# Kernel tuning notes

Measured on AMD Instinct MI355X. Metric: run time of the kernel, lower is better.

## Reference

```python
import jax, jax.numpy as jnp
import numpy as np

B, N, D, U, S = 32, 1024, 2, 64, 2


def setup_inputs() -> dict:
    key = jax.random.key(0)
    ks = jax.random.split(key, 8)
    scale = 1.0 / np.sqrt(N)  # keep diffusion outputs in a sane range
    inputs = jax.random.normal(ks[0], (B, N, D), jnp.float32)
    supports = jax.random.normal(ks[1], (B, N, N, S), jnp.float32) * scale
    h_prev = jax.random.normal(ks[2], (B, N * U), jnp.float32)
    rows = (D + U) * (S + 1)  # 198
    wscale = 1.0 / np.sqrt(rows)
    r_kernel = jax.random.normal(ks[3], (rows, U), jnp.float32) * wscale
    u_kernel = jax.random.normal(ks[4], (rows, U), jnp.float32) * wscale
    c_kernel = jax.random.normal(ks[5], (rows, U), jnp.float32) * wscale
    zeros = jnp.zeros((U,), jnp.float32)
    return {"inputs": inputs, "supports": supports, "h_prev": h_prev,
            "r_kernel": r_kernel, "r_bias": zeros,
            "u_kernel": u_kernel, "u_bias": zeros,
            "c_kernel": c_kernel, "c_bias": zeros}


def _diff_conv(x_in, supports, state, kernel, bias):
    # x_in: (B,N,D), state: (B, N*U) -> output (B, N*U)
    b, n, _ = x_in.shape
    u = kernel.shape[1]
    x0 = jnp.concatenate([x_in, state.reshape(b, n, u)], axis=-1)  # (B,N,F)
    # batched graph diffusion for all S supports at once: (B,N,N,S)x(B,N,F)->(B,N,F,S)
    xm = jnp.einsum('bijs,bjf->bifs', supports, x0)
    x = jnp.concatenate([x0[..., None], xm], axis=-1)  # (B,N,F,M) matches tf stack+transpose order
    x = x.reshape(b * n, -1) @ kernel + bias  # (B*N, U)
    return x.reshape(b, n * u)


def reference(inputs, supports, h_prev, r_kernel, r_bias, u_kernel, u_bias, c_kernel, c_bias):
    r = jax.nn.sigmoid(_diff_conv(inputs, supports, h_prev, r_kernel, r_bias))
    u = jax.nn.sigmoid(_diff_conv(inputs, supports, h_prev, u_kernel, u_bias))
    c = jnp.tanh(_diff_conv(inputs, supports, r * h_prev, c_kernel, c_bias))
    h = u * h_prev + (1.0 - u) * c
    return h
```

## Files before the change

kernel.cpp:

```cpp
#include <hip/hip_runtime.h>
#include <hip/hip_bf16.h>

namespace {

constexpr int kN  = 1024;
constexpr int kU  = 64;
constexpr int kFP = 80;
constexpr int kXR = 132;

typedef __attribute__((ext_vector_type(4))) float f32x4;
typedef __attribute__((ext_vector_type(8))) short sv8;
typedef unsigned int u32;
typedef unsigned short u16;

__device__ __forceinline__ u32 pack_bf2(float a, float b) {
  __hip_bfloat16 ha = __float2bfloat16(a);
  __hip_bfloat16 hb = __float2bfloat16(b);
  u16 ua = *reinterpret_cast<u16*>(&ha);
  u16 ub = *reinterpret_cast<u16*>(&hb);
  return (u32)ua | ((u32)ub << 16);
}

__device__ __forceinline__ u16 bf16bits(float a) {
  __hip_bfloat16 h = __float2bfloat16(a);
  return *reinterpret_cast<u16*>(&h);
}

__device__ __forceinline__ float bflo(u32 v) {
  u32 x = v << 16;
  return *reinterpret_cast<float*>(&x);
}
__device__ __forceinline__ float bfhi(u32 v) {
  u32 x = v & 0xffff0000u;
  return *reinterpret_cast<float*>(&x);
}

__device__ __forceinline__ void gl16(const void* g, void* l) {
  __builtin_amdgcn_global_load_lds(
      (const __attribute__((address_space(1))) u32*)g,
      (__attribute__((address_space(3))) u32*)l, 16, 0, 0);
}

__global__ __launch_bounds__(256) void build_x0t(
    const float* __restrict__ inputs, const float* __restrict__ h_prev,
    __hip_bfloat16* __restrict__ x0t, __hip_bfloat16* __restrict__ x0tc) {
  const int bx = blockIdx.x;
  const int b  = bx >> 4;
  const int n0 = (bx & 15) * 64;
  const int t  = threadIdx.x;

  __shared__ float hp[64][65];

  const float* hpg = h_prev + (size_t)b * kN * kU + (size_t)n0 * kU;
#pragma unroll
  for (int r = 0; r < 16; ++r) {
    int idx = t + (r << 8);
    hp[idx >> 6][idx & 63] = hpg[idx];
  }
  __syncthreads();

  {
    int u = t >> 2, g = t & 3;
    __hip_bfloat16* dst = x0t + ((size_t)b * kFP + 2 + u) * kN + n0 + g * 16;
#pragma unroll
    for (int k = 0; k < 16; ++k) dst[k] = __float2bfloat16(hp[g * 16 + k][u]);
  }

  if (t < 128) {
    int d = t & 1, nn = t >> 1;
    float v = inputs[((size_t)b * kN + n0 + nn) * 2 + d];
    __hip_bfloat16 bv = __float2bfloat16(v);
    x0t [((size_t)b * kFP + d) * kN + n0 + nn] = bv;
    x0tc[((size_t)b * kFP + d) * kN + n0 + nn] = bv;
  } else {
    int i2 = t - 128;
    __hip_bfloat16 z = __float2bfloat16(0.0f);
#pragma unroll
    for (int r = 0; r < 7; ++r) {
      int idx = i2 + r * 128;
      int row = 66 + (idx >> 6), nn = idx & 63;
      x0t [((size_t)b * kFP + row) * kN + n0 + nn] = z;
      x0tc[((size_t)b * kFP + row) * kN + n0 + nn] = z;
    }
  }
}

__global__ __launch_bounds__(512, 4) void einsum_diff(
    const float* __restrict__ sup, const __hip_bfloat16* __restrict__ x0t,
    u16* __restrict__ xfeat) {
  const int bx = blockIdx.x;
  const int wk = (bx & 7) * 64 + (bx >> 3);
  const int b  = wk >> 4;
  const int i0 = (wk & 15) << 6;
  const int t    = threadIdx.x;
  const int lane = t & 63;
  const int w    = t >> 6;
  const int q    = lane >> 4;
  const int lm   = lane & 15;
  const int s    = w & 1;
  const int ih   = w >> 1;

  __shared__ u16 Af[2][2][2][4][64][8];
  __shared__ u16 Xf[2][10][64][8];

  f32x4 acc[5];
#pragma unroll
  for (int n = 0; n < 5; ++n) acc[n] = (f32x4){0.f, 0.f, 0.f, 0.f};

  const float* sbase = sup + ((size_t)b * kN + i0) * (kN * 2);
  const u16* xg = reinterpret_cast<const u16*>(x0t) + (size_t)b * kFP * kN;

  const int ii = t >> 3, jb = t & 7;
  const float* aSrc = sbase + (size_t)ii * (kN * 2) + jb * 16;
  const int ksA = jb >> 2, q2 = jb & 3;
  const int ihhA = ii >> 4, lm2 = ii & 15;
  const int aOff = ksA * 4096 + ihhA * 1024 +
                   ((((q2 * 16 + lm2) * 16)) ^ (q2 << 4) ^ (ksA << 6));
  char* const afBase = (char*)&Af[0][0][0][0][0][0];

  const int seg1 = w;
  const int seg2 = w + 8;
  const u16* xs1;
  const u16* xs2 = nullptr;
  {
    int k1 = seg1 / 5, n1 = seg1 % 5;
    xs1 = xg + (size_t)(n1 * 16 + lm) * kN + k1 * 32 + q * 8;
    if (w < 2) {
      int k2 = seg2 / 5, n2 = seg2 % 5;
      xs2 = xg + (size_t)(n2 * 16 + lm) * kN + k2 * 32 + q * 8;
    }
  }

  float4 R[4];

  auto dmaX = [&](int nb, int T) {
    int jo = T * 64;
    gl16(xs1 + jo, &Xf[nb][seg1][0][0]);
    if (w < 2) gl16(xs2 + jo, &Xf[nb][seg2][0][0]);
  };

  auto loadA = [&](int T) {
    const float* p = aSrc + T * 128;
    R[0] = *reinterpret_cast<const float4*>(p);
    R[1] = *reinterpret_cast<const float4*>(p + 4);
    R[2] = *reinterpret_cast<const float4*>(p + 8);
    R[3] = *reinterpret_cast<const float4*>(p + 12);
  };

  auto packWrite = [&](int nb) {
    u32 p0[4], p1[4];
#pragma unroll
    for (int r = 0; r < 4; ++r) {
      p0[r] = pack_bf2(R[r].x, R[r].z);
      p1[r] = pack_bf2(R[r].y, R[r].w);
    }
    char* base = afBase + nb * 16384 + aOff;
    *reinterpret_cast<uint4*>(base)        = *reinterpret_cast<uint4*>(p0);
    *reinterpret_cast<uint4*>(base + 8192) = *reinterpret_cast<uint4*>(p1);
  };

  auto compute = [&](int cb_) {
#pragma unroll
    for (int ks = 0; ks < 2; ++ks) {
      const char* ab = afBase + cb_ * 16384 + s * 8192 + ks * 4096 + ih * 1024;
      sv8 a = *reinterpret_cast<const sv8*>(
          ab + ((((q * 16 + lm) * 16)) ^ (q << 4) ^ (ks << 6)));
#pragma unroll
      for (int n = 0; n < 5; ++n) {
        sv8 xb = *reinterpret_cast<const sv8*>(&Xf[cb_][ks * 5 + n][lane][0]);
        acc[n] = __builtin_amdgcn_mfma_f32_16x16x32_bf16(a, xb, acc[n], 0, 0, 0);
      }
    }
  };

  dmaX(0, 0);
  loadA(0);
  asm volatile("s_waitcnt vmcnt(0)" ::: "memory");
  packWrite(0);
  asm volatile("s_waitcnt lgkmcnt(0)" ::: "memory");
  __builtin_amdgcn_s_barrier();
  __builtin_amdgcn_sched_barrier(0);

#pragma unroll 1
  for (int T = 0; T < 15; ++T) {
    const int nb = (T + 1) & 1;
    dmaX(nb, T + 1);
    loadA(T + 1);
    compute(T & 1);
    asm volatile("s_waitcnt vmcnt(0)" ::: "memory");
    packWrite(nb);
    asm volatile("s_waitcnt lgkmcnt(0)" ::: "memory");
    __builtin_amdgcn_s_barrier();
    __builtin_amdgcn_sched_barrier(0);
  }
  compute(1);
  __syncthreads();

  u16* ep = (u16*)afBase;
#pragma unroll
  for (int n = 0; n < 5; ++n) {
    int f = n * 16 + lm;
    if (f < 66) {
#pragma unroll
      for (int r = 0; r < 4; ++r) {
        int row = ih * 16 + q * 4 + r;
        ep[row * 136 + s * 66 + f] = bf16bits(acc[n][r]);
      }
    }
  }
  __syncthreads();
  const u32* ep32 = (const u32*)afBase;
  u32* og = reinterpret_cast<u32*>(xfeat) + ((size_t)b * kN + i0) * 66;
#pragma unroll 1
  for (int g = t; g < 4224; g += 512) {
    int row = g / 66, c = g - row * 66;
    og[g] = ep32[row * 68 + c];
  }
}

__global__ __launch_bounds__(256) void gates_ru(
    const u16* __restrict__ xfeat, const float* __restrict__ rk,
    const float* __restrict__ rbias, const float* __restrict__ uk,
    const float* __restrict__ ubias, const float* __restrict__ inputs,
    const float* __restrict__ h_prev, float* __restrict__ u_buf,
    __hip_bfloat16* __restrict__ x0tc) {
  const int row0 = blockIdx.x * 32;
  const int b = row0 >> 10, n0 = row0 & 1023;
  const int t = threadIdx.x;
  __shared__ float xm[32][134];
  __shared__ float x0s[32][66];

  {
    const u32* xsrc = reinterpret_cast<const u32*>(xfeat) + (size_t)row0 * 66;
#pragma unroll 1
    for (int g = t; g < 2112; g += 256) {
      int row = g / 66, c = g - row * 66;
      u32 v = xsrc[g];
      xm[row][c * 2]     = bflo(v);
      xm[row][c * 2 + 1] = bfhi(v);
    }
  }
#pragma unroll
  for (int r2 = 0; r2 < 8; ++r2) {
    int idx = t + (r2 << 8);
    int rw = idx >> 6, u = idx & 63;
    x0s[rw][2 + u] = h_prev[(size_t)(row0 + rw) * kU + u];
  }
  if (t < 64) x0s[t >> 1][t & 1] = inputs[(size_t)row0 * 2 + t];
  __syncthreads();

  const int cu = t & 15;
  const int rw = (t >> 4) * 2;
  float ar[2][4] = {{0.f,0.f,0.f,0.f},{0.f,0.f,0.f,0.f}};
  float au[2][4] = {{0.f,0.f,0.f,0.f},{0.f,0.f,0.f,0.f}};

#pragma unroll 4
  for (int f = 0; f < 66; ++f) {
    float4 vr = *reinterpret_cast<const float4*>(rk + (size_t)(f * 3) * kU + cu * 4);
    float4 vu = *reinterpret_cast<const float4*>(uk + (size_t)(f * 3) * kU + cu * 4);
    float a0 = x0s[rw][f], a1 = x0s[rw + 1][f];
    ar[0][0] += a0 * vr.x; ar[0][1] += a0 * vr.y; ar[0][2] += a0 * vr.z; ar[0][3] += a0 * vr.w;
    ar[1][0] += a1 * vr.x; ar[1][1] += a1 * vr.y; ar[1][2] += a1 * vr.z; ar[1][3] += a1 * vr.w;
    au[0][0] += a0 * vu.x; au[0][1] += a0 * vu.y; au[0][2] += a0 * vu.z; au[0][3] += a0 * vu.w;
    au[1][0] += a1 * vu.x; au[1][1] += a1 * vu.y; au[1][2] += a1 * vu.z; au[1][3] += a1 * vu.w;
  }
#pragma unroll
  for (int m = 1; m <= 2; ++m) {
#pragma unroll 4
    for (int f = 0; f < 66; ++f) {
      float4 vr = *reinterpret_cast<const float4*>(rk + (size_t)(f * 3 + m) * kU + cu * 4);
      float4 vu = *reinterpret_cast<const float4*>(uk + (size_t)(f * 3 + m) * kU + cu * 4);
      float a0 = xm[rw][(m - 1) * 66 + f], a1 = xm[rw + 1][(m - 1) * 66 + f];
      ar[0][0] += a0 * vr.x; ar[0][1] += a0 * vr.y; ar[0][2] += a0 * vr.z; ar[0][3] += a0 * vr.w;
      ar[1][0] += a1 * vr.x; ar[1][1] += a1 * vr.y; ar[1][2] += a1 * vr.z; ar[1][3] += a1 * vr.w;
      au[0][0] += a0 * vu.x; au[0][1] += a0 * vu.y; au[0][2] += a0 * vu.z; au[0][3] += a0 * vu.w;
      au[1][0] += a1 * vu.x; au[1][1] += a1 * vu.y; au[1][2] += a1 * vu.z; au[1][3] += a1 * vu.w;
    }
  }

#pragma unroll
  for (int rr = 0; rr < 2; ++rr) {
    int grow = row0 + rw + rr;
    int n = n0 + rw + rr;
#pragma unroll
    for (int j = 0; j < 4; ++j) {
      int u = cu * 4 + j;
      float rv = 1.f / (1.f + __expf(-(ar[rr][j] + rbias[u])));
      float uv = 1.f / (1.f + __expf(-(au[rr][j] + ubias[u])));
      u_buf[(size_t)grow * kU + u] = uv;
      float rh = rv * h_prev[(size_t)grow * kU + u];
      x0tc[((size_t)b * kFP + 2 + u) * kN + n] = __float2bfloat16(rh);
    }
  }
}

__global__ __launch_bounds__(256) void gate_c_final(
    const u16* __restrict__ xfeat, const float* __restrict__ ck,
    const float* __restrict__ cbias, const float* __restrict__ inputs,
    const __hip_bfloat16* __restrict__ x0tc, const float* __restrict__ h_prev,
    const float* __restrict__ u_buf, float* __restrict__ out) {
  const int row0 = blockIdx.x * 32;
  const int b = row0 >> 10, n0 = row0 & 1023;
  const int t = threadIdx.x;
  __shared__ float xm[32][134];
  __shared__ float x0c[32][66];

  {
    const u32* xsrc = reinterpret_cast<const u32*>(xfeat) + (size_t)row0 * 66;
#pragma unroll 1
    for (int g = t; g < 2112; g += 256) {
      int row = g / 66, c = g - row * 66;
      u32 v = xsrc[g];
      xm[row][c * 2]     = bflo(v);
      xm[row][c * 2 + 1] = bfhi(v);
    }
  }
#pragma unroll
  for (int r2 = 0; r2 < 8; ++r2) {
    int idx = t + (r2 << 8);
    int u = idx >> 5, nn = idx & 31;
    x0c[nn][2 + u] =
        __bfloat162float(x0tc[((size_t)b * kFP + 2 + u) * kN + n0 + nn]);
  }
  if (t < 64) x0c[t >> 1][t & 1] = inputs[(size_t)row0 * 2 + t];
  __syncthreads();

  const int cu = t & 15;
  const int rw = (t >> 4) * 2;
  float ac[2][4] = {{0.f,0.f,0.f,0.f},{0.f,0.f,0.f,0.f}};

#pragma unroll 4
  for (int f = 0; f < 66; ++f) {
    float4 vc = *reinterpret_cast<const float4*>(ck + (size_t)(f * 3) * kU + cu * 4);
    float a0 = x0c[rw][f], a1 = x0c[rw + 1][f];
    ac[0][0] += a0 * vc.x; ac[0][1] += a0 * vc.y; ac[0][2] += a0 * vc.z; ac[0][3] += a0 * vc.w;
    ac[1][0] += a1 * vc.x; ac[1][1] += a1 * vc.y; ac[1][2] += a1 * vc.z; ac[1][3] += a1 * vc.w;
  }
#pragma unroll
  for (int m = 1; m <= 2; ++m) {
#pragma unroll 4
    for (int f = 0; f < 66; ++f) {
      float4 vc = *reinterpret_cast<const float4*>(ck + (size_t)(f * 3 + m) * kU + cu * 4);
      float a0 = xm[rw][(m - 1) * 66 + f], a1 = xm[rw + 1][(m - 1) * 66 + f];
      ac[0][0] += a0 * vc.x; ac[0][1] += a0 * vc.y; ac[0][2] += a0 * vc.z; ac[0][3] += a0 * vc.w;
      ac[1][0] += a1 * vc.x; ac[1][1] += a1 * vc.y; ac[1][2] += a1 * vc.z; ac[1][3] += a1 * vc.w;
    }
  }

#pragma unroll
  for (int rr = 0; rr < 2; ++rr) {
    int grow = row0 + rw + rr;
#pragma unroll
    for (int j = 0; j < 4; ++j) {
      int u = cu * 4 + j;
      float cv = tanhf(ac[rr][j] + cbias[u]);
      float uv = u_buf[(size_t)grow * kU + u];
      float hp = h_prev[(size_t)grow * kU + u];
      out[(size_t)grow * kU + u] = uv * hp + (1.f - uv) * cv;
    }
  }
}

}

extern "C" void kernel_launch(void* const* d_in, const int* in_sizes, int n_in,
                              void* d_out, int out_size, void* d_ws, size_t ws_size,
                              hipStream_t stream) {
  const float* inputs = (const float*)d_in[0];
  const float* sup    = (const float*)d_in[1];
  const float* h_prev = (const float*)d_in[2];
  const float* rk     = (const float*)d_in[3];
  const float* rbias  = (const float*)d_in[4];
  const float* uk     = (const float*)d_in[5];
  const float* ubias  = (const float*)d_in[6];
  const float* ck     = (const float*)d_in[7];
  const float* cbias  = (const float*)d_in[8];
  float* out = (float*)d_out;

  char* ws = (char*)d_ws;
  __hip_bfloat16* x0t   = (__hip_bfloat16*)(ws);
  __hip_bfloat16* x0tc  = (__hip_bfloat16*)(ws + 5242880);
  u16*            xfeat = (u16*)(ws + 10485760);
  float*          u_buf = (float*)(ws + 19136512);

  hipLaunchKernelGGL(build_x0t, dim3(512), dim3(256), 0, stream,
                     inputs, h_prev, x0t, x0tc);
  hipLaunchKernelGGL(einsum_diff, dim3(512), dim3(512), 0, stream,
                     sup, x0t, xfeat);
  hipLaunchKernelGGL(gates_ru, dim3(1024), dim3(256), 0, stream,
                     xfeat, rk, rbias, uk, ubias, inputs, h_prev, u_buf, x0tc);
  hipLaunchKernelGGL(einsum_diff, dim3(512), dim3(512), 0, stream,
                     sup, x0tc, xfeat);
  hipLaunchKernelGGL(gate_c_final, dim3(1024), dim3(256), 0, stream,
                     xfeat, ck, cbias, inputs, x0tc, h_prev, u_buf, out);
}
```

Before: 232.6 us.

## Load einsum operands straight into registers and drop LDS staging and barriers

Rewrites the diffusion einsum kernel so each wave loads its own rows of supports and the x0 tile directly from global memory into registers, double-buffered across k-steps, and converts them to bf16 MFMA fragments in registers. Both supports go through the same wave, which removes the shared-memory staging of A and X and the per-iteration barriers. Blocks shrink to 256 threads, and each wave now covers 16 rows with two accumulator sets. The trade-off is that neighbouring waves no longer share X through LDS, so X is re-read redundantly from cache. Register pressure also rises, which may lower occupancy.

New measurement: 266.4 us. +14.5%, slower.

```diff
diff --git a/kernel.cpp b/kernel.cpp
--- a/kernel.cpp
+++ b/kernel.cpp
@@ -6,10 +6,10 @@
 constexpr int kN  = 1024;
 constexpr int kU  = 64;
 constexpr int kFP = 80;
-constexpr int kXR = 132;
 
 typedef __attribute__((ext_vector_type(4))) float f32x4;
 typedef __attribute__((ext_vector_type(8))) short sv8;
+typedef __attribute__((ext_vector_type(4))) unsigned u32x4;
 typedef unsigned int u32;
 typedef unsigned short u16;
 
@@ -33,12 +33,6 @@
 __device__ __forceinline__ float bfhi(u32 v) {
   u32 x = v & 0xffff0000u;
   return *reinterpret_cast<float*>(&x);
-}
-
-__device__ __forceinline__ void gl16(const void* g, void* l) {
-  __builtin_amdgcn_global_load_lds(
-      (const __attribute__((address_space(1))) u32*)g,
-      (__attribute__((address_space(3))) u32*)l, 16, 0, 0);
 }
 
 __global__ __launch_bounds__(256) void build_x0t(
@@ -85,134 +79,100 @@
   }
 }
 
-__global__ __launch_bounds__(512, 4) void einsum_diff(
+__global__ __launch_bounds__(256, 2) void einsum_diff(
     const float* __restrict__ sup, const __hip_bfloat16* __restrict__ x0t,
     u16* __restrict__ xfeat) {
   const int bx = blockIdx.x;
   const int wk = (bx & 7) * 64 + (bx >> 3);
-  const int b  = wk >> 4;
-  const int i0 = (wk & 15) << 6;
   const int t    = threadIdx.x;
   const int lane = t & 63;
   const int w    = t >> 6;
   const int q    = lane >> 4;
   const int lm   = lane & 15;
-  const int s    = w & 1;
-  const int ih   = w >> 1;
-
-  __shared__ u16 Af[2][2][2][4][64][8];
-  __shared__ u16 Xf[2][10][64][8];
-
-  f32x4 acc[5];
-#pragma unroll
-  for (int n = 0; n < 5; ++n) acc[n] = (f32x4){0.f, 0.f, 0.f, 0.f};
-
-  const float* sbase = sup + ((size_t)b * kN + i0) * (kN * 2);
-  const u16* xg = reinterpret_cast<const u16*>(x0t) + (size_t)b * kFP * kN;
-
-  const int ii = t >> 3, jb = t & 7;
-  const float* aSrc = sbase + (size_t)ii * (kN * 2) + jb * 16;
-  const int ksA = jb >> 2, q2 = jb & 3;
-  const int ihhA = ii >> 4, lm2 = ii & 15;
-  const int aOff = ksA * 4096 + ihhA * 1024 +
-                   ((((q2 * 16 + lm2) * 16)) ^ (q2 << 4) ^ (ksA << 6));
-  char* const afBase = (char*)&Af[0][0][0][0][0][0];
-
-  const int seg1 = w;
-  const int seg2 = w + 8;
-  const u16* xs1;
-  const u16* xs2 = nullptr;
-  {
-    int k1 = seg1 / 5, n1 = seg1 % 5;
-    xs1 = xg + (size_t)(n1 * 16 + lm) * kN + k1 * 32 + q * 8;
-    if (w < 2) {
-      int k2 = seg2 / 5, n2 = seg2 % 5;
-      xs2 = xg + (size_t)(n2 * 16 + lm) * kN + k2 * 32 + q * 8;
-    }
-  }
-
-  float4 R[4];
-
-  auto dmaX = [&](int nb, int T) {
-    int jo = T * 64;
-    gl16(xs1 + jo, &Xf[nb][seg1][0][0]);
-    if (w < 2) gl16(xs2 + jo, &Xf[nb][seg2][0][0]);
+
+  const int gw  = wk * 4 + w;
+  const int b   = gw >> 6;
+  const int i0w = (gw & 63) * 16;
+  const int i0b = ((wk * 4) & 63) * 16;
+
+  __shared__ u16 ep[64][136];
+
+  f32x4 acc[2][5];
+#pragma unroll
+  for (int s_ = 0; s_ < 2; ++s_)
+#pragma unroll
+    for (int n = 0; n < 5; ++n) acc[s_][n] = (f32x4){0.f, 0.f, 0.f, 0.f};
+
+  const float* aB = sup + ((size_t)b * kN + i0w + lm) * (kN * 2) + q * 16;
+  const u16* xg2 = reinterpret_cast<const u16*>(x0t) +
+                   (size_t)b * kFP * kN + (size_t)lm * kN + q * 8;
+
+  sv8   XP[10], XQ[10];
+  float4 AP[8], AQ[8];
+
+  auto issue = [&](sv8 (&X)[10], float4 (&A)[8], int T) {
+#pragma unroll
+    for (int ks = 0; ks < 2; ++ks) {
+#pragma unroll
+      for (int r = 0; r < 4; ++r)
+        A[ks * 4 + r] = *reinterpret_cast<const float4*>(
+            aB + T * 128 + ks * 64 + r * 4);
+#pragma unroll
+      for (int n = 0; n < 5; ++n)
+        X[ks * 5 + n] = *reinterpret_cast<const sv8*>(
+            xg2 + (size_t)n * 16 * kN + ks * 32 + T * 64);
+    }
   };
 
-  auto loadA = [&](int T) {
-    const float* p = aSrc + T * 128;
-    R[0] = *reinterpret_cast<const float4*>(p);
-    R[1] = *reinterpret_cast<const float4*>(p + 4);
-    R[2] = *reinterpret_cast<const float4*>(p + 8);
-    R[3] = *reinterpret_cast<const float4*>(p + 12);
+  auto step = [&](const sv8 (&X)[10], const float4 (&A)[8]) {
+#pragma unroll
+    for (int ks = 0; ks < 2; ++ks) {
+      u32 w0[4], w1[4];
+#pragma unroll
+      for (int r = 0; r < 4; ++r) {
+        w0[r] = pack_bf2(A[ks * 4 + r].x, A[ks * 4 + r].z);
+        w1[r] = pack_bf2(A[ks * 4 + r].y, A[ks * 4 + r].w);
+      }
+      sv8 a0 = __builtin_bit_cast(sv8, (u32x4){w0[0], w0[1], w0[2], w0[3]});
+      sv8 a1 = __builtin_bit_cast(sv8, (u32x4){w1[0], w1[1], w1[2], w1[3]});
+#pragma unroll
+      for (int n = 0; n < 5; ++n) {
+        acc[0][n] = __builtin_amdgcn_mfma_f32_16x16x32_bf16(a0, X[ks * 5 + n], acc[0][n], 0, 0, 0);
+        acc[1][n] = __builtin_amdgcn_mfma_f32_16x16x32_bf16(a1, X[ks * 5 + n], acc[1][n], 0, 0, 0);
+      }
+    }
   };
 
-  auto packWrite = [&](int nb) {
-    u32 p0[4], p1[4];
-#pragma unroll
-    for (int r = 0; r < 4; ++r) {
-      p0[r] = pack_bf2(R[r].x, R[r].z);
-      p1[r] = pack_bf2(R[r].y, R[r].w);
-    }
-    char* base = afBase + nb * 16384 + aOff;
-    *reinterpret_cast<uint4*>(base)        = *reinterpret_cast<uint4*>(p0);
-    *reinterpret_cast<uint4*>(base + 8192) = *reinterpret_cast<uint4*>(p1);
-  };
-
-  auto compute = [&](int cb_) {
-#pragma unroll
-    for (int ks = 0; ks < 2; ++ks) {
-      const char* ab = afBase + cb_ * 16384 + s * 8192 + ks * 4096 + ih * 1024;
-      sv8 a = *reinterpret_cast<const sv8*>(
-          ab + ((((q * 16 + lm) * 16)) ^ (q << 4) ^ (ks << 6)));
-#pragma unroll
-      for (int n = 0; n < 5; ++n) {
-        sv8 xb = *reinterpret_cast<const sv8*>(&Xf[cb_][ks * 5 + n][lane][0]);
-        acc[n] = __builtin_amdgcn_mfma_f32_16x16x32_bf16(a, xb, acc[n], 0, 0, 0);
+  issue(XP, AP, 0);
+#pragma unroll 1
+  for (int T2 = 0; T2 < 8; ++T2) {
+    const int T = T2 * 2;
+    issue(XQ, AQ, T + 1);
+    step(XP, AP);
+    if (T + 2 < 16) issue(XP, AP, T + 2);
+    step(XQ, AQ);
+  }
+
+  __syncthreads();
+#pragma unroll
+  for (int s_ = 0; s_ < 2; ++s_) {
+#pragma unroll
+    for (int n = 0; n < 5; ++n) {
+      int f = n * 16 + lm;
+      if (f < 66) {
+#pragma unroll
+        for (int r = 0; r < 4; ++r) {
+          int row = w * 16 + q * 4 + r;
+          ep[row][s_ * 66 + f] = bf16bits(acc[s_][n][r]);
+        }
       }
     }
-  };
-
-  dmaX(0, 0);
-  loadA(0);
-  asm volatile("s_waitcnt vmcnt(0)" ::: "memory");
-  packWrite(0);
-  asm volatile("s_waitcnt lgkmcnt(0)" ::: "memory");
-  __builtin_amdgcn_s_barrier();
-  __builtin_amdgcn_sched_barrier(0);
-
+  }
+  __syncthreads();
+  const u32* ep32 = reinterpret_cast<const u32*>(&ep[0][0]);
+  u32* og = reinterpret_cast<u32*>(xfeat) + ((size_t)b * kN + i0b) * 66;
 #pragma unroll 1
-  for (int T = 0; T < 15; ++T) {
-    const int nb = (T + 1) & 1;
-    dmaX(nb, T + 1);
-    loadA(T + 1);
-    compute(T & 1);
-    asm volatile("s_waitcnt vmcnt(0)" ::: "memory");
-    packWrite(nb);
-    asm volatile("s_waitcnt lgkmcnt(0)" ::: "memory");
-    __builtin_amdgcn_s_barrier();
-    __builtin_amdgcn_sched_barrier(0);
-  }
-  compute(1);
-  __syncthreads();
-
-  u16* ep = (u16*)afBase;
-#pragma unroll
-  for (int n = 0; n < 5; ++n) {
-    int f = n * 16 + lm;
-    if (f < 66) {
-#pragma unroll
-      for (int r = 0; r < 4; ++r) {
-        int row = ih * 16 + q * 4 + r;
-        ep[row * 136 + s * 66 + f] = bf16bits(acc[n][r]);
-      }
-    }
-  }
-  __syncthreads();
-  const u32* ep32 = (const u32*)afBase;
-  u32* og = reinterpret_cast<u32*>(xfeat) + ((size_t)b * kN + i0) * 66;
-#pragma unroll 1
-  for (int g = t; g < 4224; g += 512) {
+  for (int g = t; g < 4224; g += 256) {
     int row = g / 66, c = g - row * 66;
     og[g] = ep32[row * 68 + c];
   }
@@ -385,11 +345,11 @@
 
   hipLaunchKernelGGL(build_x0t, dim3(512), dim3(256), 0, stream,
                      inputs, h_prev, x0t, x0tc);
-  hipLaunchKernelGGL(einsum_diff, dim3(512), dim3(512), 0, stream,
+  hipLaunchKernelGGL(einsum_diff, dim3(512), dim3(256), 0, stream,
                      sup, x0t, xfeat);
   hipLaunchKernelGGL(gates_ru, dim3(1024), dim3(256), 0, stream,
                      xfeat, rk, rbias, uk, ubias, inputs, h_prev, u_buf, x0tc);
-  hipLaunchKernelGGL(einsum_diff, dim3(512), dim3(512), 0, stream,
+  hipLaunchKernelGGL(einsum_diff, dim3(512), dim3(256), 0, stream,
                      sup, x0tc, xfeat);
   hipLaunchKernelGGL(gate_c_final, dim3(1024), dim3(256), 0, stream,
                      xfeat, ck, cbias, inputs, x0tc, h_prev, u_buf, out);
```

## Single-buffer einsum tiles with doubled K-step and restructured load/compute pipeline

Applied to the files above, without the earlier changes.

Reworks the diffusion einsum main loop to process 128-wide K chunks (8 iterations instead of 16) using single-buffered LDS tiles for both the support matrix and the x0 operand, with a new XOR swizzle layout. Global loads of the next support tile are issued before compute, but the LDS writes and X DMA now happen after a barrier, so compute and LDS fill no longer overlap via double buffering. Fewer barriers and larger per-thread loads are intended to cut loop overhead, at the cost of doubled register use for the prefetched rows and less overlap between compute and stores.

Measured after the change: 247.0 us. 6.2% more time.

```diff
diff --git a/kernel.cpp b/kernel.cpp
--- a/kernel.cpp
+++ b/kernel.cpp
@@ -6,7 +6,6 @@
 constexpr int kN  = 1024;
 constexpr int kU  = 64;
 constexpr int kFP = 80;
-constexpr int kXR = 132;
 
 typedef __attribute__((ext_vector_type(4))) float f32x4;
 typedef __attribute__((ext_vector_type(8))) short sv8;
@@ -100,103 +99,101 @@
   const int s    = w & 1;
   const int ih   = w >> 1;
 
-  __shared__ u16 Af[2][2][2][4][64][8];
-  __shared__ u16 Xf[2][10][64][8];
+  __shared__ u16 Af[2][4][4][64][8];
+  __shared__ u16 Xf[20][64][8];
 
   f32x4 acc[5];
 #pragma unroll
   for (int n = 0; n < 5; ++n) acc[n] = (f32x4){0.f, 0.f, 0.f, 0.f};
 
-  const float* sbase = sup + ((size_t)b * kN + i0) * (kN * 2);
+  const int ii = t >> 3, p = t & 7;
+  const float* aSrc = sup + ((size_t)b * kN + i0 + ii) * (kN * 2) + p * 32;
+  const int ksA  = p >> 1;
+  const int q0   = (p & 1) * 2;
+  const int ihhA = ii >> 4;
+  const int lmA  = (ii & 15) ^ (ksA << 1);
+
   const u16* xg = reinterpret_cast<const u16*>(x0t) + (size_t)b * kFP * kN;
-
-  const int ii = t >> 3, jb = t & 7;
-  const float* aSrc = sbase + (size_t)ii * (kN * 2) + jb * 16;
-  const int ksA = jb >> 2, q2 = jb & 3;
-  const int ihhA = ii >> 4, lm2 = ii & 15;
-  const int aOff = ksA * 4096 + ihhA * 1024 +
-                   ((((q2 * 16 + lm2) * 16)) ^ (q2 << 4) ^ (ksA << 6));
-  char* const afBase = (char*)&Af[0][0][0][0][0][0];
-
-  const int seg1 = w;
-  const int seg2 = w + 8;
-  const u16* xs1;
-  const u16* xs2 = nullptr;
-  {
-    int k1 = seg1 / 5, n1 = seg1 % 5;
-    xs1 = xg + (size_t)(n1 * 16 + lm) * kN + k1 * 32 + q * 8;
-    if (w < 2) {
-      int k2 = seg2 / 5, n2 = seg2 % 5;
-      xs2 = xg + (size_t)(n2 * 16 + lm) * kN + k2 * 32 + q * 8;
-    }
-  }
-
-  float4 R[4];
-
-  auto dmaX = [&](int nb, int T) {
-    int jo = T * 64;
-    gl16(xs1 + jo, &Xf[nb][seg1][0][0]);
-    if (w < 2) gl16(xs2 + jo, &Xf[nb][seg2][0][0]);
+  const int segA_ = w, segB_ = w + 8, segC_ = w + 16;
+  const u16* xs1 = xg + (size_t)((segA_ % 5) * 16 + lm) * kN + (segA_ / 5) * 32 + q * 8;
+  const u16* xs2 = xg + (size_t)((segB_ % 5) * 16 + lm) * kN + (segB_ / 5) * 32 + q * 8;
+  const u16* xs3 = (w < 4)
+      ? xg + (size_t)((segC_ % 5) * 16 + lm) * kN + (segC_ / 5) * 32 + q * 8
+      : nullptr;
+
+  auto dmaX = [&](int T) {
+    int jo = T * 128;
+    gl16(xs1 + jo, &Xf[segA_][0][0]);
+    gl16(xs2 + jo, &Xf[segB_][0][0]);
+    if (w < 4) gl16(xs3 + jo, &Xf[segC_][0][0]);
   };
 
+  float4 R[8];
   auto loadA = [&](int T) {
-    const float* p = aSrc + T * 128;
-    R[0] = *reinterpret_cast<const float4*>(p);
-    R[1] = *reinterpret_cast<const float4*>(p + 4);
-    R[2] = *reinterpret_cast<const float4*>(p + 8);
-    R[3] = *reinterpret_cast<const float4*>(p + 12);
+    const float* pp = aSrc + (size_t)T * 256;
+#pragma unroll
+    for (int r = 0; r < 8; ++r)
+      R[r] = *reinterpret_cast<const float4*>(pp + r * 4);
   };
 
-  auto packWrite = [&](int nb) {
-    u32 p0[4], p1[4];
-#pragma unroll
-    for (int r = 0; r < 4; ++r) {
-      p0[r] = pack_bf2(R[r].x, R[r].z);
-      p1[r] = pack_bf2(R[r].y, R[r].w);
-    }
-    char* base = afBase + nb * 16384 + aOff;
-    *reinterpret_cast<uint4*>(base)        = *reinterpret_cast<uint4*>(p0);
-    *reinterpret_cast<uint4*>(base + 8192) = *reinterpret_cast<uint4*>(p1);
+  auto writeA = [&]() {
+    u32 w0[8], w1[8];
+#pragma unroll
+    for (int k = 0; k < 8; ++k) {
+      w0[k] = pack_bf2(R[k].x, R[k].z);
+      w1[k] = pack_bf2(R[k].y, R[k].w);
+    }
+    uint4* d;
+    d = reinterpret_cast<uint4*>(&Af[0][ksA][ihhA][q0 * 16 + lmA][0]);
+    *d = (uint4){w0[0], w0[1], w0[2], w0[3]};
+    d = reinterpret_cast<uint4*>(&Af[0][ksA][ihhA][(q0 + 1) * 16 + lmA][0]);
+    *d = (uint4){w0[4], w0[5], w0[6], w0[7]};
+    d = reinterpret_cast<uint4*>(&Af[1][ksA][ihhA][q0 * 16 + lmA][0]);
+    *d = (uint4){w1[0], w1[1], w1[2], w1[3]};
+    d = reinterpret_cast<uint4*>(&Af[1][ksA][ihhA][(q0 + 1) * 16 + lmA][0]);
+    *d = (uint4){w1[4], w1[5], w1[6], w1[7]};
   };
 
-  auto compute = [&](int cb_) {
-#pragma unroll
-    for (int ks = 0; ks < 2; ++ks) {
-      const char* ab = afBase + cb_ * 16384 + s * 8192 + ks * 4096 + ih * 1024;
+  auto compute = [&]() {
+#pragma unroll
+    for (int ks = 0; ks < 4; ++ks) {
       sv8 a = *reinterpret_cast<const sv8*>(
-          ab + ((((q * 16 + lm) * 16)) ^ (q << 4) ^ (ks << 6)));
+          &Af[s][ks][ih][q * 16 + (lm ^ (ks << 1))][0]);
 #pragma unroll
       for (int n = 0; n < 5; ++n) {
-        sv8 xb = *reinterpret_cast<const sv8*>(&Xf[cb_][ks * 5 + n][lane][0]);
+        sv8 xb = *reinterpret_cast<const sv8*>(&Xf[ks * 5 + n][lane][0]);
         acc[n] = __builtin_amdgcn_mfma_f32_16x16x32_bf16(a, xb, acc[n], 0, 0, 0);
       }
     }
   };
 
-  dmaX(0, 0);
   loadA(0);
+  dmaX(0);
   asm volatile("s_waitcnt vmcnt(0)" ::: "memory");
-  packWrite(0);
+  writeA();
   asm volatile("s_waitcnt lgkmcnt(0)" ::: "memory");
   __builtin_amdgcn_s_barrier();
   __builtin_amdgcn_sched_barrier(0);
 
 #pragma unroll 1
-  for (int T = 0; T < 15; ++T) {
-    const int nb = (T + 1) & 1;
-    dmaX(nb, T + 1);
-    loadA(T + 1);
-    compute(T & 1);
-    asm volatile("s_waitcnt vmcnt(0)" ::: "memory");
-    packWrite(nb);
-    asm volatile("s_waitcnt lgkmcnt(0)" ::: "memory");
+  for (int T = 0; T < 8; ++T) {
+    if (T < 7) loadA(T + 1);
+    compute();
     __builtin_amdgcn_s_barrier();
     __builtin_amdgcn_sched_barrier(0);
-  }
-  compute(1);
-  __syncthreads();
-
-  u16* ep = (u16*)afBase;
+    if (T < 7) {
+      dmaX(T + 1);
+      if (w < 4) { asm volatile("s_waitcnt vmcnt(3)" ::: "memory"); }
+      else       { asm volatile("s_waitcnt vmcnt(2)" ::: "memory"); }
+      writeA();
+      asm volatile("s_waitcnt vmcnt(0) lgkmcnt(0)" ::: "memory");
+      __builtin_amdgcn_s_barrier();
+      __builtin_amdgcn_sched_barrier(0);
+    }
+  }
+
+  __builtin_amdgcn_s_barrier();
+  u16* ep = (u16*)&Af[0][0][0][0][0];
 #pragma unroll
   for (int n = 0; n < 5; ++n) {
     int f = n * 16 + lm;
@@ -209,7 +206,7 @@
     }
   }
   __syncthreads();
-  const u32* ep32 = (const u32*)afBase;
+  const u32* ep32 = reinterpret_cast<const u32*>(ep);
   u32* og = reinterpret_cast<u32*>(xfeat) + ((size_t)b * kN + i0) * 66;
 #pragma unroll 1
   for (int g = t; g < 4224; g += 512) {
```

## Pre-convert supports to bf16 in a separate pass reused by both einsums

Applied to the files above, without the earlier changes.

Adds a streaming kernel that converts the fp32 supports tensor to packed bf16 once per call. Both diffusion einsum passes then read the half-size bf16 copy and only repack bits into LDS, with no float conversion. This aims to cut the per-einsum read traffic and conversion work. The cost is an extra full read of supports plus a 128 MB write and an additional launch.

After: 223.3 us. -4.0%, faster.

```diff
diff --git a/kernel.cpp b/kernel.cpp
--- a/kernel.cpp
+++ b/kernel.cpp
@@ -6,7 +6,6 @@
 constexpr int kN  = 1024;
 constexpr int kU  = 64;
 constexpr int kFP = 80;
-constexpr int kXR = 132;
 
 typedef __attribute__((ext_vector_type(4))) float f32x4;
 typedef __attribute__((ext_vector_type(8))) short sv8;
@@ -39,6 +38,21 @@
   __builtin_amdgcn_global_load_lds(
       (const __attribute__((address_space(1))) u32*)g,
       (__attribute__((address_space(3))) u32*)l, 16, 0, 0);
+}
+
+__global__ __launch_bounds__(256) void convert_sup(
+    const f32x4* __restrict__ sup4, uint2* __restrict__ outb) {
+  const size_t n4 = (size_t)16 * 1024 * 1024;
+  size_t idx = (size_t)blockIdx.x * 256 + threadIdx.x;
+  const size_t stride = (size_t)gridDim.x * 256;
+#pragma unroll 1
+  for (; idx < n4; idx += stride) {
+    f32x4 v = __builtin_nontemporal_load(sup4 + idx);
+    uint2 o;
+    o.x = pack_bf2(v[0], v[1]);
+    o.y = pack_bf2(v[2], v[3]);
+    outb[idx] = o;
+  }
 }
 
 __global__ __launch_bounds__(256) void build_x0t(
@@ -86,7 +100,7 @@
 }
 
 __global__ __launch_bounds__(512, 4) void einsum_diff(
-    const float* __restrict__ sup, const __hip_bfloat16* __restrict__ x0t,
+    const u32* __restrict__ supb, const __hip_bfloat16* __restrict__ x0t,
     u16* __restrict__ xfeat) {
   const int bx = blockIdx.x;
   const int wk = (bx & 7) * 64 + (bx >> 3);
@@ -107,31 +121,26 @@
 #pragma unroll
   for (int n = 0; n < 5; ++n) acc[n] = (f32x4){0.f, 0.f, 0.f, 0.f};
 
-  const float* sbase = sup + ((size_t)b * kN + i0) * (kN * 2);
+  const u32* sb = supb + ((size_t)b * kN + i0) * kN;
   const u16* xg = reinterpret_cast<const u16*>(x0t) + (size_t)b * kFP * kN;
 
   const int ii = t >> 3, jb = t & 7;
-  const float* aSrc = sbase + (size_t)ii * (kN * 2) + jb * 16;
+  const u32* aSrc = sb + (size_t)ii * kN + jb * 8;
   const int ksA = jb >> 2, q2 = jb & 3;
   const int ihhA = ii >> 4, lm2 = ii & 15;
   const int aOff = ksA * 4096 + ihhA * 1024 +
-                   ((((q2 * 16 + lm2) * 16)) ^ (q2 << 4) ^ (ksA << 6));
+                   (((q2 * 16 + lm2) * 16) ^ (q2 << 4) ^ (ksA << 6));
   char* const afBase = (char*)&Af[0][0][0][0][0][0];
 
   const int seg1 = w;
   const int seg2 = w + 8;
-  const u16* xs1;
-  const u16* xs2 = nullptr;
-  {
-    int k1 = seg1 / 5, n1 = seg1 % 5;
-    xs1 = xg + (size_t)(n1 * 16 + lm) * kN + k1 * 32 + q * 8;
-    if (w < 2) {
-      int k2 = seg2 / 5, n2 = seg2 % 5;
-      xs2 = xg + (size_t)(n2 * 16 + lm) * kN + k2 * 32 + q * 8;
-    }
-  }
-
-  float4 R[4];
+  const u16* xs1 =
+      xg + (size_t)((seg1 % 5) * 16 + lm) * kN + (seg1 / 5) * 32 + q * 8;
+  const u16* xs2 = (w < 2)
+      ? xg + (size_t)((seg2 % 5) * 16 + lm) * kN + (seg2 / 5) * 32 + q * 8
+      : nullptr;
+
+  uint4 W1, W2;
 
   auto dmaX = [&](int nb, int T) {
     int jo = T * 64;
@@ -140,23 +149,24 @@
   };
 
   auto loadA = [&](int T) {
-    const float* p = aSrc + T * 128;
-    R[0] = *reinterpret_cast<const float4*>(p);
-    R[1] = *reinterpret_cast<const float4*>(p + 4);
-    R[2] = *reinterpret_cast<const float4*>(p + 8);
-    R[3] = *reinterpret_cast<const float4*>(p + 12);
+    const u32* p = aSrc + T * 64;
+    W1 = *reinterpret_cast<const uint4*>(p);
+    W2 = *reinterpret_cast<const uint4*>(p + 4);
   };
 
   auto packWrite = [&](int nb) {
     u32 p0[4], p1[4];
-#pragma unroll
-    for (int r = 0; r < 4; ++r) {
-      p0[r] = pack_bf2(R[r].x, R[r].z);
-      p1[r] = pack_bf2(R[r].y, R[r].w);
-    }
+    p0[0] = (W1.x & 0xffffu) | (W1.y << 16);
+    p0[1] = (W1.z & 0xffffu) | (W1.w << 16);
+    p0[2] = (W2.x & 0xffffu) | (W2.y << 16);
+    p0[3] = (W2.z & 0xffffu) | (W2.w << 16);
+    p1[0] = (W1.x >> 16) | (W1.y & 0xffff0000u);
+    p1[1] = (W1.z >> 16) | (W1.w & 0xffff0000u);
+    p1[2] = (W2.x >> 16) | (W2.y & 0xffff0000u);
+    p1[3] = (W2.z >> 16) | (W2.w & 0xffff0000u);
     char* base = afBase + nb * 16384 + aOff;
-    *reinterpret_cast<uint4*>(base)        = *reinterpret_cast<uint4*>(p0);
-    *reinterpret_cast<uint4*>(base + 8192) = *reinterpret_cast<uint4*>(p1);
+    *reinterpret_cast<uint4*>(base)        = (uint4){p0[0], p0[1], p0[2], p0[3]};
+    *reinterpret_cast<uint4*>(base + 8192) = (uint4){p1[0], p1[1], p1[2], p1[3]};
   };
 
   auto compute = [&](int cb_) {
@@ -164,7 +174,7 @@
     for (int ks = 0; ks < 2; ++ks) {
       const char* ab = afBase + cb_ * 16384 + s * 8192 + ks * 4096 + ih * 1024;
       sv8 a = *reinterpret_cast<const sv8*>(
-          ab + ((((q * 16 + lm) * 16)) ^ (q << 4) ^ (ks << 6)));
+          ab + (((q * 16 + lm) * 16) ^ (q << 4) ^ (ks << 6)));
 #pragma unroll
       for (int n = 0; n < 5; ++n) {
         sv8 xb = *reinterpret_cast<const sv8*>(&Xf[cb_][ks * 5 + n][lane][0]);
@@ -209,7 +219,7 @@
     }
   }
   __syncthreads();
-  const u32* ep32 = (const u32*)afBase;
+  const u32* ep32 = reinterpret_cast<const u32*>(ep);
   u32* og = reinterpret_cast<u32*>(xfeat) + ((size_t)b * kN + i0) * 66;
 #pragma unroll 1
   for (int g = t; g < 4224; g += 512) {
@@ -382,15 +392,18 @@
   __hip_bfloat16* x0tc  = (__hip_bfloat16*)(ws + 5242880);
   u16*            xfeat = (u16*)(ws + 10485760);
   float*          u_buf = (float*)(ws + 19136512);
-
+  u32*            supb  = (u32*)(ws + 27525120);
+
+  hipLaunchKernelGGL(convert_sup, dim3(4096), dim3(256), 0, stream,
+                     (const f32x4*)sup, (uint2*)supb);
   hipLaunchKernelGGL(build_x0t, dim3(512), dim3(256), 0, stream,
                      inputs, h_prev, x0t, x0tc);
   hipLaunchKernelGGL(einsum_diff, dim3(512), dim3(512), 0, stream,
-                     sup, x0t, xfeat);
+                     supb, x0t, xfeat);
   hipLaunchKernelGGL(gates_ru, dim3(1024), dim3(256), 0, stream,
                      xfeat, rk, rbias, uk, ubias, inputs, h_prev, u_buf, x0tc);
   hipLaunchKernelGGL(einsum_diff, dim3(512), dim3(512), 0, stream,
-                     sup, x0tc, xfeat);
+                     supb, x0tc, xfeat);
   hipLaunchKernelGGL(gate_c_final, dim3(1024), dim3(256), 0, stream,
                      xfeat, ck, cbias, inputs, x0tc, h_prev, u_buf, out);
 }
```
